# Optimization experiments

Measured on AMD Instinct MI355X. Metric: run time of the kernel, lower is better.

Reference implementation:

```python
import jax, jax.numpy as jnp
import numpy as np

EPS = 1e-3   # Keras BatchNormalization default epsilon
DT = 0.2     # dt
K = 2        # PDE time steps


def _bn(x, p):
    # p: [4, C] = (gamma, beta, moving_mean, moving_var); inference-mode BN
    g, b, m, v = p
    return g * (x - m) * jax.lax.rsqrt(v + EPS) + b


def _dw(x, k):
    # depthwise 3x3 'same' conv; x: NHWC, k: (3,3,1,C)
    return jax.lax.conv_general_dilated(
        x, k, window_strides=(1, 1), padding='SAME',
        dimension_numbers=('NHWC', 'HWIO', 'NHWC'),
        feature_group_count=x.shape[-1])


def setup_inputs() -> dict:
    key = jax.random.key(0)
    ks = jax.random.split(key, 10)
    B, H, W, C = 16, 128, 128, 64
    x = jax.random.normal(ks[0], (B, H, W, C), jnp.float32)

    def kern(k):
        return jax.random.normal(k, (3, 3, 1, C), jnp.float32) * 0.1

    def bnp(k):
        k1, k2, k3, k4 = jax.random.split(k, 4)
        return jnp.stack([
            1.0 + 0.1 * jax.random.normal(k1, (C,), jnp.float32),  # gamma
            0.1 * jax.random.normal(k2, (C,), jnp.float32),        # beta
            0.1 * jax.random.normal(k3, (C,), jnp.float32),        # moving_mean
            0.5 + jax.random.uniform(k4, (C,), jnp.float32),       # moving_var > 0
        ])

    return {
        's0': x,
        'kg': kern(ks[1]), 'kg1': kern(ks[2]),
        'kDx': kern(ks[3]), 'kDy': kern(ks[4]),
        'bng': bnp(ks[5]), 'bng1': bnp(ks[6]),
        'bnDx': bnp(ks[7]), 'bnDy': bnp(ks[8]),
        'bn_out': bnp(ks[9]),
    }


def reference(s0, kg, kg1, kDx, kDy, bng, bng1, bnDx, bnDy, bn_out):
    # init_h is identity ('default' block_type); stride==1, in_chs==out_chs
    f = s0
    h = f
    h0 = f
    g = jax.nn.relu(_bn(_dw(h, kg), bng))
    g1 = jax.nn.relu(_bn(_dw(h, kg1), bng1))
    Dx = jax.nn.relu(_bn(_dw(h, kDx), bnDx))
    Dy = jax.nn.relu(_bn(_dw(h, kDy), bnDy))
    # dx = dy = 1; rolls on axis 2 and 3 exactly as in the TF code (NHWC)
    ux = 0.5 * (jnp.roll(g, 1, axis=2) - jnp.roll(g, -1, axis=2))
    vy = 0.5 * (jnp.roll(g1, 1, axis=3) - jnp.roll(g1, -1, axis=3))
    Ax = g * DT
    Ay = g1 * DT
    Bx = Dx * DT
    By = Dy * DT
    E = (ux + vy) * DT
    D = 1.0 / (1.0 + 2.0 * Bx + 2.0 * By)
    for _ in range(K):
        prev_h = h
        h = D * ((1.0 - 2.0 * Bx - 2.0 * By) * h0
                 - 2.0 * E * h
                 + (-Ax + 2.0 * Bx) * jnp.roll(h, 1, axis=2)
                 + (Ax + 2.0 * Bx) * jnp.roll(h, -1, axis=2)
                 + (-Ay + 2.0 * By) * jnp.roll(h, 1, axis=3)
                 + (Ay + 2.0 * By) * jnp.roll(h, -1, axis=3))
        h = h + D * (2.0 * DT) * f
        h0 = prev_h
    return jax.nn.relu(_bn(h, bn_out))
```

## Files before the change

kernel.cpp:

```cpp
#include <hip/hip_runtime.h>

#define HH 128
#define WW 128
#define CC 64
#define BS 512
#define RS (WW * CC)
#define NPT 4
#define NSTRIP 32

typedef float f4 __attribute__((ext_vector_type(4)));

static __device__ __forceinline__ f4 vload(const float* __restrict__ p) {
    return *reinterpret_cast<const f4*>(p);
}
static __device__ __forceinline__ void vstore(float* p, f4 v) {
    *reinterpret_cast<f4*>(p) = v;
}
static __device__ __forceinline__ f4 vrelu(f4 a) {
    f4 r;
    #pragma unroll
    for (int i = 0; i < 4; ++i) r[i] = fmaxf(a[i], 0.f);
    return r;
}
static __device__ __forceinline__ f4 vrsq_eps(f4 a) {
    f4 r;
    #pragma unroll
    for (int i = 0; i < 4; ++i) r[i] = __builtin_amdgcn_rsqf(a[i] + 1e-3f);
    return r;
}
static __device__ __forceinline__ f4 vrcp(f4 a) {
    f4 r;
    #pragma unroll
    for (int i = 0; i < 4; ++i) r[i] = __builtin_amdgcn_rcpf(a[i]);
    return r;
}

static __device__ __forceinline__ void croll(f4 v, int lm, int lp, f4& cm, f4& cp) {
    const float m3 = __shfl(v.w, lm);
    const float p0 = __shfl(v.x, lp);
    cm.x = m3;  cm.y = v.x; cm.z = v.y; cm.w = v.z;
    cp.x = v.y; cp.y = v.z; cp.z = v.w; cp.w = p0;
}

__global__ __launch_bounds__(BS) void diffusion_fused(
    const float* __restrict__ s0,
    const float* __restrict__ kg,  const float* __restrict__ kg1,
    const float* __restrict__ kDx, const float* __restrict__ kDy,
    const float* __restrict__ bng,  const float* __restrict__ bng1,
    const float* __restrict__ bnDx, const float* __restrict__ bnDy,
    const float* __restrict__ bn_out,
    float* __restrict__ out)
{
    __shared__ float GH[2 * NSTRIP * CC];
    __shared__ float FH[2 * NSTRIP * CC];
    __shared__ float HHb[2 * NSTRIP * CC];

    const int t  = threadIdx.x;
    const int cq = t & 15;
    const int c4 = cq << 2;
    const int s  = t >> 4;
    const int w0 = s << 2;
    const int l  = t & 63;
    const int lm = (l & 48) | ((l + 15) & 15);
    const int lp = (l & 48) | ((l + 1)  & 15);
    const int sl = (s + NSTRIP - 1) & (NSTRIP - 1);
    const int sr = (s + 1) & (NSTRIP - 1);

    const int bid = blockIdx.x;
    const int bh  = ((bid & 7) << 8) | (bid >> 3);
    const int hrow = bh & (HH - 1);
    const long rowbase = (long)bh * RS;
    const bool rowm = (hrow > 0), rowp = (hrow < HH - 1);

    const bool zl = (s == 0), zr = (s == NSTRIP - 1);
    int oc[6];
    oc[0] = (zl ? 0 : (w0 - 1)) * CC + c4;
    #pragma unroll
    for (int j = 1; j <= 4; ++j) oc[j] = (w0 + j - 1) * CC + c4;
    oc[5] = (zr ? (WW - 1) : (w0 + 4)) * CC + c4;

    #define BNFOLD(P, S, B, SC) { \
        const f4 ga  = vload((P) + c4);        \
        const f4 be  = vload((P) + 64 + c4);   \
        const f4 mu  = vload((P) + 128 + c4);  \
        const f4 va  = vload((P) + 192 + c4);  \
        const f4 sc0 = ga * vrsq_eps(va);      \
        S = sc0 * (SC);                        \
        B = (be - mu * sc0) * (SC); }

    f4 s_g, b_g, s_g1, b_g1;
    BNFOLD(bng,  s_g,  b_g,  1.0f);
    BNFOLD(bng1, s_g1, b_g1, 1.0f);

    f4 ag[NPT], ag1[NPT];
    #pragma unroll
    for (int i = 0; i < NPT; ++i) { ag[i] = (f4)0.f; ag1[i] = (f4)0.f; }

    #pragma unroll
    for (int dh = -1; dh <= 1; ++dh) {
        if (dh == -1 && !rowm) continue;
        if (dh ==  1 && !rowp) continue;
        const float* rp = s0 + rowbase + (long)dh * RS;
        f4 in[6];
        #pragma unroll
        for (int j = 0; j < 6; ++j) in[j] = vload(rp + oc[j]);
        if (zl) in[0] = (f4)0.f;
        if (zr) in[5] = (f4)0.f;
        #pragma unroll
        for (int dw = 0; dw < 3; ++dw) {
            const int kk = (dh + 1) * 3 + dw;
            const f4 wg  = vload(kg  + kk * CC + c4);
            const f4 wg1 = vload(kg1 + kk * CC + c4);
            #pragma unroll
            for (int i = 0; i < NPT; ++i) {
                ag[i]  += in[dw + i] * wg;
                ag1[i] += in[dw + i] * wg1;
            }
        }
    }

    f4 g[NPT], g1[NPT];
    #pragma unroll
    for (int i = 0; i < NPT; ++i) {
        g[i]  = vrelu(ag[i]  * s_g  + b_g );
        g1[i] = vrelu(ag1[i] * s_g1 + b_g1);
    }
    vstore(&GH[s * CC + c4],            g[0]);
    vstore(&GH[(NSTRIP + s) * CC + c4], g[NPT - 1]);

    f4 s_dx, b_dx, s_dy, b_dy;
    BNFOLD(bnDx, s_dx, b_dx, 0.4f);
    BNFOLD(bnDy, s_dy, b_dy, 0.4f);

    f4 adx[NPT], ady[NPT], h[NPT];
    #pragma unroll
    for (int i = 0; i < NPT; ++i) { adx[i] = (f4)0.f; ady[i] = (f4)0.f; }

    #pragma unroll
    for (int dh = -1; dh <= 1; ++dh) {
        if (dh == -1 && !rowm) continue;
        if (dh ==  1 && !rowp) continue;
        const float* rp = s0 + rowbase + (long)dh * RS;
        f4 in[6];
        #pragma unroll
        for (int j = 0; j < 6; ++j) in[j] = vload(rp + oc[j]);
        if (zl) in[0] = (f4)0.f;
        if (zr) in[5] = (f4)0.f;
        if (dh == 0) {
            #pragma unroll
            for (int i = 0; i < NPT; ++i) h[i] = in[i + 1];
        }
        #pragma unroll
        for (int dw = 0; dw < 3; ++dw) {
            const int kk = (dh + 1) * 3 + dw;
            const f4 wdx = vload(kDx + kk * CC + c4);
            const f4 wdy = vload(kDy + kk * CC + c4);
            #pragma unroll
            for (int i = 0; i < NPT; ++i) {
                adx[i] += in[dw + i] * wdx;
                ady[i] += in[dw + i] * wdy;
            }
        }
    }
    vstore(&FH[s * CC + c4],            h[0]);
    vstore(&FH[(NSTRIP + s) * CC + c4], h[NPT - 1]);

    f4 cWm[NPT], cWp[NPT], cCm[NPT], cCp[NPT], A0[NPT], PqD[NPT], uv[NPT];
    #pragma unroll
    for (int i = 0; i < NPT; ++i) {
        const f4 tbx = vrelu(adx[i] * s_dx + b_dx);
        const f4 tby = vrelu(ady[i] * s_dy + b_dy);
        const f4 Dv  = vrcp((f4)1.f + tbx + tby);
        const f4 Ax  = g[i]  * 0.2f;
        const f4 Ay  = g1[i] * 0.2f;
        cWm[i] = Dv * (tbx - Ax);
        cWp[i] = Dv * (tbx + Ax);
        cCm[i] = Dv * (tby - Ay);
        cCp[i] = Dv * (tby + Ay);
        A0[i]  = Dv * h[i] * ((f4)1.4f - tbx - tby);
        PqD[i] = Dv * (-0.4f);
        f4 cm, cp;
        croll(g1[i], lm, lp, cm, cp);
        uv[i] = 0.5f * (cm - cp);
    }
    uv[0] -= 0.5f * g[1];
    uv[1] += 0.5f * (g[0] - g[2]);
    uv[2] += 0.5f * (g[1] - g[3]);
    uv[3] += 0.5f * g[2];
    __syncthreads();

    f4 cE[NPT];
    {
        const f4 gL = vload(&GH[(NSTRIP + sl) * CC + c4]);
        const f4 gR = vload(&GH[sr * CC + c4]);
        cE[0] = PqD[0] * (uv[0] + 0.5f * gL);
        cE[1] = PqD[1] * uv[1];
        cE[2] = PqD[2] * uv[2];
        cE[3] = PqD[3] * (uv[3] - 0.5f * gR);
    }

    f4 hn[NPT];
    {
        const f4 hL = vload(&FH[(NSTRIP + sl) * CC + c4]);
        const f4 hR = vload(&FH[sr * CC + c4]);
        #pragma unroll
        for (int i = 0; i < NPT; ++i) {
            const f4 hm = (i == 0)       ? hL : h[i - 1];
            const f4 hp = (i == NPT - 1) ? hR : h[i + 1];
            f4 cm, cp;
            croll(h[i], lm, lp, cm, cp);
            hn[i] = A0[i] + cE[i] * h[i] + cWm[i] * hm + cWp[i] * hp
                  + cCm[i] * cm + cCp[i] * cp;
        }
    }
    vstore(&HHb[s * CC + c4],            hn[0]);
    vstore(&HHb[(NSTRIP + s) * CC + c4], hn[NPT - 1]);
    __syncthreads();

    f4 h2v[NPT];
    {
        const f4 hL = vload(&HHb[(NSTRIP + sl) * CC + c4]);
        const f4 hR = vload(&HHb[sr * CC + c4]);
        #pragma unroll
        for (int i = 0; i < NPT; ++i) {
            const f4 hm = (i == 0)       ? hL : hn[i - 1];
            const f4 hp = (i == NPT - 1) ? hR : hn[i + 1];
            f4 cm, cp;
            croll(hn[i], lm, lp, cm, cp);
            h2v[i] = A0[i] + cE[i] * hn[i] + cWm[i] * hm + cWp[i] * hp
                   + cCm[i] * cm + cCp[i] * cp;
        }
    }

    f4 s_o, b_o;
    BNFOLD(bn_out, s_o, b_o, 1.0f);
    #undef BNFOLD
    #pragma unroll
    for (int i = 0; i < NPT; ++i)
        vstore(out + rowbase + oc[i + 1], vrelu(h2v[i] * s_o + b_o));
}

extern "C" void kernel_launch(void* const* d_in, const int* in_sizes, int n_in,
                              void* d_out, int out_size, void* d_ws, size_t ws_size,
                              hipStream_t stream) {
    const float* s0   = (const float*)d_in[0];
    const float* kg   = (const float*)d_in[1];
    const float* kg1  = (const float*)d_in[2];
    const float* kDx  = (const float*)d_in[3];
    const float* kDy  = (const float*)d_in[4];
    const float* bng  = (const float*)d_in[5];
    const float* bng1 = (const float*)d_in[6];
    const float* bnDx = (const float*)d_in[7];
    const float* bnDy = (const float*)d_in[8];
    const float* bno  = (const float*)d_in[9];
    float* out = (float*)d_out;

    dim3 grid(16 * 128);
    dim3 block(BS);
    diffusion_fused<<<grid, block, 0, stream>>>(
        s0, kg, kg1, kDx, kDy, bng, bng1, bnDx, bnDy, bno, out);
}
```

Measured before the change: 171.3 us.

## Process 8 rows per block with LDS ring buffer and async global-to-LDS staging

Each block now handles eight consecutive image rows instead of one, staging input rows into a three-slot LDS ring through global_load_lds so each input row is fetched once per block rather than three times. Conv weights and folded BN parameters are cached in LDS once per block, and all four depthwise convs are merged into a single pass. This cuts redundant global reads and per-block setup. In exchange it adds per-row barriers, much larger LDS use and a grid of only 256 blocks, which may limit occupancy and latency hiding.

```diff
diff --git a/kernel.cpp b/kernel.cpp
--- a/kernel.cpp
+++ b/kernel.cpp
@@ -7,10 +7,11 @@
 #define RS (WW * CC)
 #define NPT 4
 #define NSTRIP 32
+#define ROWS 8
 
 typedef float f4 __attribute__((ext_vector_type(4)));
 
-static __device__ __forceinline__ f4 vload(const float* __restrict__ p) {
+static __device__ __forceinline__ f4 vload(const float* p) {
     return *reinterpret_cast<const f4*>(p);
 }
 static __device__ __forceinline__ void vstore(float* p, f4 v) {
@@ -34,12 +35,58 @@
     for (int i = 0; i < 4; ++i) r[i] = __builtin_amdgcn_rcpf(a[i]);
     return r;
 }
-
 static __device__ __forceinline__ void croll(f4 v, int lm, int lp, f4& cm, f4& cp) {
     const float m3 = __shfl(v.w, lm);
     const float p0 = __shfl(v.x, lp);
     cm.x = m3;  cm.y = v.x; cm.z = v.y; cm.w = v.z;
     cp.x = v.y; cp.y = v.z; cp.z = v.w; cp.w = p0;
+}
+
+static __device__ __forceinline__ void gld_lds16(const float* g, float* l) {
+    __builtin_amdgcn_global_load_lds(
+        (const __attribute__((address_space(1))) void*)g,
+        (__attribute__((address_space(3))) void*)l,
+        16, 0, 0);
+}
+static __device__ __forceinline__ void stage_row(const float* g, float* l,
+                                                 int wv, int ln) {
+    #pragma unroll
+    for (int it = 0; it < 4; ++it) {
+        const int off = (it * 8 + wv) * 256;
+        gld_lds16(g + off + ln * 4, l + off);
+    }
+}
+
+template<bool CENTER>
+static __device__ __forceinline__ void conv_taps(
+    const float* R, const float* WTS, int kbase, const int* oc,
+    bool zl, bool zr, int c4,
+    f4* ag, f4* ag1, f4* adx, f4* ady, f4* h)
+{
+    f4 in[6];
+    #pragma unroll
+    for (int jj = 0; jj < 6; ++jj) in[jj] = vload(R + oc[jj]);
+    if (zl) in[0] = (f4)0.f;
+    if (zr) in[5] = (f4)0.f;
+    if (CENTER) {
+        #pragma unroll
+        for (int i = 0; i < NPT; ++i) h[i] = in[i + 1];
+    }
+    #pragma unroll
+    for (int dw = 0; dw < 3; ++dw) {
+        const int kk = kbase + dw;
+        const f4 wg  = vload(WTS + (0 * 9 + kk) * CC + c4);
+        const f4 wg1 = vload(WTS + (1 * 9 + kk) * CC + c4);
+        const f4 wdx = vload(WTS + (2 * 9 + kk) * CC + c4);
+        const f4 wdy = vload(WTS + (3 * 9 + kk) * CC + c4);
+        #pragma unroll
+        for (int i = 0; i < NPT; ++i) {
+            ag[i]  += in[dw + i] * wg;
+            ag1[i] += in[dw + i] * wg1;
+            adx[i] += in[dw + i] * wdx;
+            ady[i] += in[dw + i] * wdy;
+        }
+    }
 }
 
 __global__ __launch_bounds__(BS) void diffusion_fused(
@@ -51,9 +98,11 @@
     const float* __restrict__ bn_out,
     float* __restrict__ out)
 {
-    __shared__ float GH[2 * NSTRIP * CC];
-    __shared__ float FH[2 * NSTRIP * CC];
-    __shared__ float HHb[2 * NSTRIP * CC];
+    __shared__ __attribute__((aligned(16))) float ring[3][RS];
+    __shared__ __attribute__((aligned(16))) float GH[2 * NSTRIP * CC];
+    __shared__ __attribute__((aligned(16))) float HHb[2 * NSTRIP * CC];
+    __shared__ __attribute__((aligned(16))) float WTS[4 * 9 * CC];
+    __shared__ __attribute__((aligned(16))) float BNF[10 * CC];
 
     const int t  = threadIdx.x;
     const int cq = t & 15;
@@ -61,16 +110,16 @@
     const int s  = t >> 4;
     const int w0 = s << 2;
     const int l  = t & 63;
+    const int wv = t >> 6;
     const int lm = (l & 48) | ((l + 15) & 15);
     const int lp = (l & 48) | ((l + 1)  & 15);
     const int sl = (s + NSTRIP - 1) & (NSTRIP - 1);
     const int sr = (s + 1) & (NSTRIP - 1);
 
     const int bid = blockIdx.x;
-    const int bh  = ((bid & 7) << 8) | (bid >> 3);
-    const int hrow = bh & (HH - 1);
-    const long rowbase = (long)bh * RS;
-    const bool rowm = (hrow > 0), rowp = (hrow < HH - 1);
+    const int img = bid >> 4;
+    const int r0  = (bid & 15) << 3;
+    const long imgbase = (long)img * HH * RS;
 
     const bool zl = (s == 0), zr = (s == NSTRIP - 1);
     int oc[6];
@@ -78,166 +127,151 @@
     #pragma unroll
     for (int j = 1; j <= 4; ++j) oc[j] = (w0 + j - 1) * CC + c4;
     oc[5] = (zr ? (WW - 1) : (w0 + 4)) * CC + c4;
-
-    #define BNFOLD(P, S, B, SC) { \
-        const f4 ga  = vload((P) + c4);        \
-        const f4 be  = vload((P) + 64 + c4);   \
-        const f4 mu  = vload((P) + 128 + c4);  \
-        const f4 va  = vload((P) + 192 + c4);  \
-        const f4 sc0 = ga * vrsq_eps(va);      \
-        S = sc0 * (SC);                        \
-        B = (be - mu * sc0) * (SC); }
-
-    f4 s_g, b_g, s_g1, b_g1;
-    BNFOLD(bng,  s_g,  b_g,  1.0f);
-    BNFOLD(bng1, s_g1, b_g1, 1.0f);
-
-    f4 ag[NPT], ag1[NPT];
-    #pragma unroll
-    for (int i = 0; i < NPT; ++i) { ag[i] = (f4)0.f; ag1[i] = (f4)0.f; }
-
-    #pragma unroll
-    for (int dh = -1; dh <= 1; ++dh) {
-        if (dh == -1 && !rowm) continue;
-        if (dh ==  1 && !rowp) continue;
-        const float* rp = s0 + rowbase + (long)dh * RS;
-        f4 in[6];
-        #pragma unroll
-        for (int j = 0; j < 6; ++j) in[j] = vload(rp + oc[j]);
-        if (zl) in[0] = (f4)0.f;
-        if (zr) in[5] = (f4)0.f;
-        #pragma unroll
-        for (int dw = 0; dw < 3; ++dw) {
-            const int kk = (dh + 1) * 3 + dw;
-            const f4 wg  = vload(kg  + kk * CC + c4);
-            const f4 wg1 = vload(kg1 + kk * CC + c4);
+    const int wmo = ((w0 - 1) & (WW - 1)) * CC + c4;
+    const int wpo = ((w0 + 4) & (WW - 1)) * CC + c4;
+
+    if (r0 > 0)
+        stage_row(s0 + imgbase + (long)(r0 - 1) * RS, ring[(r0 - 1) % 3], wv, l);
+    stage_row(s0 + imgbase + (long)r0 * RS,       ring[r0 % 3],       wv, l);
+    stage_row(s0 + imgbase + (long)(r0 + 1) * RS, ring[(r0 + 1) % 3], wv, l);
+
+    {
+        const float* wsrc[4] = { kg, kg1, kDx, kDy };
+        #pragma unroll
+        for (int base = 0; base < 576; base += BS) {
+            const int slot = base + t;
+            if (slot < 576) {
+                const int q   = slot / 144;
+                const int rem = slot - q * 144;
+                const int kk  = rem >> 4;
+                const int cc4 = (rem & 15) << 2;
+                vstore(&WTS[(q * 9 + kk) * CC + cc4], vload(wsrc[q] + kk * CC + cc4));
+            }
+        }
+    }
+    if (s == 0) {
+        #define BNF1(P, K, SC) { \
+            const f4 ga = vload((P) + c4);       const f4 be = vload((P) + 64 + c4);  \
+            const f4 mu = vload((P) + 128 + c4); const f4 va = vload((P) + 192 + c4); \
+            const f4 sc0 = ga * vrsq_eps(va);                                         \
+            vstore(&BNF[(2 * (K)) * CC + c4], sc0 * (SC));                            \
+            vstore(&BNF[(2 * (K) + 1) * CC + c4], (be - mu * sc0) * (SC)); }
+        BNF1(bng,    0, 1.0f);
+        BNF1(bng1,   1, 1.0f);
+        BNF1(bnDx,   2, 0.4f);
+        BNF1(bnDy,   3, 0.4f);
+        BNF1(bn_out, 4, 1.0f);
+        #undef BNF1
+    }
+    __syncthreads();
+
+    for (int j = 0; j < ROWS; ++j) {
+        const int gr = r0 + j;
+        const bool rowm = (gr > 0), rowp = (gr < HH - 1);
+        const float* Rm = ring[(gr + 2) % 3];
+        const float* Rc = ring[gr % 3];
+        const float* Rp = ring[(gr + 1) % 3];
+
+        f4 ag[NPT], ag1[NPT], adx[NPT], ady[NPT], h[NPT];
+        #pragma unroll
+        for (int i = 0; i < NPT; ++i) {
+            ag[i] = (f4)0.f; ag1[i] = (f4)0.f; adx[i] = (f4)0.f; ady[i] = (f4)0.f;
+        }
+
+        if (rowm) conv_taps<false>(Rm, WTS, 0, oc, zl, zr, c4, ag, ag1, adx, ady, h);
+        __syncthreads();
+        if (j < ROWS - 1 && gr + 2 < HH)
+            stage_row(s0 + imgbase + (long)(gr + 2) * RS, ring[(gr + 2) % 3], wv, l);
+
+        conv_taps<true >(Rc, WTS, 3, oc, zl, zr, c4, ag, ag1, adx, ady, h);
+        if (rowp) conv_taps<false>(Rp, WTS, 6, oc, zl, zr, c4, ag, ag1, adx, ady, h);
+
+        const f4 s_g  = vload(&BNF[0 * CC + c4]), b_g  = vload(&BNF[1 * CC + c4]);
+        const f4 s_g1 = vload(&BNF[2 * CC + c4]), b_g1 = vload(&BNF[3 * CC + c4]);
+        const f4 s_dx = vload(&BNF[4 * CC + c4]), b_dx = vload(&BNF[5 * CC + c4]);
+        const f4 s_dy = vload(&BNF[6 * CC + c4]), b_dy = vload(&BNF[7 * CC + c4]);
+        f4 g[NPT], g1[NPT];
+        #pragma unroll
+        for (int i = 0; i < NPT; ++i) {
+            g[i]  = vrelu(ag[i]  * s_g  + b_g );
+            g1[i] = vrelu(ag1[i] * s_g1 + b_g1);
+        }
+        vstore(&GH[s * CC + c4],            g[0]);
+        vstore(&GH[(NSTRIP + s) * CC + c4], g[NPT - 1]);
+
+        f4 cWm[NPT], cWp[NPT], cCm[NPT], cCp[NPT], A0[NPT], PqD[NPT], uv[NPT];
+        #pragma unroll
+        for (int i = 0; i < NPT; ++i) {
+            const f4 tbx = vrelu(adx[i] * s_dx + b_dx);
+            const f4 tby = vrelu(ady[i] * s_dy + b_dy);
+            const f4 Dv  = vrcp((f4)1.f + tbx + tby);
+            const f4 Ax  = g[i]  * 0.2f;
+            const f4 Ay  = g1[i] * 0.2f;
+            cWm[i] = Dv * (tbx - Ax);
+            cWp[i] = Dv * (tbx + Ax);
+            cCm[i] = Dv * (tby - Ay);
+            cCp[i] = Dv * (tby + Ay);
+            A0[i]  = Dv * h[i] * ((f4)1.4f - tbx - tby);
+            PqD[i] = Dv * (-0.4f);
+            f4 cm, cp;
+            croll(g1[i], lm, lp, cm, cp);
+            uv[i] = 0.5f * (cm - cp);
+        }
+        uv[0] -= 0.5f * g[1];
+        uv[1] += 0.5f * (g[0] - g[2]);
+        uv[2] += 0.5f * (g[1] - g[3]);
+        uv[3] += 0.5f * g[2];
+        __syncthreads();
+
+        f4 cE[NPT];
+        {
+            const f4 gL = vload(&GH[(NSTRIP + sl) * CC + c4]);
+            const f4 gR = vload(&GH[sr * CC + c4]);
+            cE[0] = PqD[0] * (uv[0] + 0.5f * gL);
+            cE[1] = PqD[1] * uv[1];
+            cE[2] = PqD[2] * uv[2];
+            cE[3] = PqD[3] * (uv[3] - 0.5f * gR);
+        }
+
+        f4 hn[NPT];
+        {
+            const f4 hL = vload(Rc + wmo);
+            const f4 hR = vload(Rc + wpo);
             #pragma unroll
             for (int i = 0; i < NPT; ++i) {
-                ag[i]  += in[dw + i] * wg;
-                ag1[i] += in[dw + i] * wg1;
+                const f4 hm = (i == 0)       ? hL : h[i - 1];
+                const f4 hp = (i == NPT - 1) ? hR : h[i + 1];
+                f4 cm, cp;
+                croll(h[i], lm, lp, cm, cp);
+                hn[i] = A0[i] + cE[i] * h[i] + cWm[i] * hm + cWp[i] * hp
+                      + cCm[i] * cm + cCp[i] * cp;
             }
         }
-    }
-
-    f4 g[NPT], g1[NPT];
-    #pragma unroll
-    for (int i = 0; i < NPT; ++i) {
-        g[i]  = vrelu(ag[i]  * s_g  + b_g );
-        g1[i] = vrelu(ag1[i] * s_g1 + b_g1);
-    }
-    vstore(&GH[s * CC + c4],            g[0]);
-    vstore(&GH[(NSTRIP + s) * CC + c4], g[NPT - 1]);
-
-    f4 s_dx, b_dx, s_dy, b_dy;
-    BNFOLD(bnDx, s_dx, b_dx, 0.4f);
-    BNFOLD(bnDy, s_dy, b_dy, 0.4f);
-
-    f4 adx[NPT], ady[NPT], h[NPT];
-    #pragma unroll
-    for (int i = 0; i < NPT; ++i) { adx[i] = (f4)0.f; ady[i] = (f4)0.f; }
-
-    #pragma unroll
-    for (int dh = -1; dh <= 1; ++dh) {
-        if (dh == -1 && !rowm) continue;
-        if (dh ==  1 && !rowp) continue;
-        const float* rp = s0 + rowbase + (long)dh * RS;
-        f4 in[6];
-        #pragma unroll
-        for (int j = 0; j < 6; ++j) in[j] = vload(rp + oc[j]);
-        if (zl) in[0] = (f4)0.f;
-        if (zr) in[5] = (f4)0.f;
-        if (dh == 0) {
-            #pragma unroll
-            for (int i = 0; i < NPT; ++i) h[i] = in[i + 1];
-        }
-        #pragma unroll
-        for (int dw = 0; dw < 3; ++dw) {
-            const int kk = (dh + 1) * 3 + dw;
-            const f4 wdx = vload(kDx + kk * CC + c4);
-            const f4 wdy = vload(kDy + kk * CC + c4);
+        vstore(&HHb[s * CC + c4],            hn[0]);
+        vstore(&HHb[(NSTRIP + s) * CC + c4], hn[NPT - 1]);
+        __syncthreads();
+
+        f4 h2v[NPT];
+        {
+            const f4 hL = vload(&HHb[(NSTRIP + sl) * CC + c4]);
+            const f4 hR = vload(&HHb[sr * CC + c4]);
             #pragma unroll
             for (int i = 0; i < NPT; ++i) {
-                adx[i] += in[dw + i] * wdx;
-                ady[i] += in[dw + i] * wdy;
+                const f4 hm = (i == 0)       ? hL : hn[i - 1];
+                const f4 hp = (i == NPT - 1) ? hR : hn[i + 1];
+                f4 cm, cp;
+                croll(hn[i], lm, lp, cm, cp);
+                h2v[i] = A0[i] + cE[i] * hn[i] + cWm[i] * hm + cWp[i] * hp
+                       + cCm[i] * cm + cCp[i] * cp;
             }
         }
-    }
-    vstore(&FH[s * CC + c4],            h[0]);
-    vstore(&FH[(NSTRIP + s) * CC + c4], h[NPT - 1]);
-
-    f4 cWm[NPT], cWp[NPT], cCm[NPT], cCp[NPT], A0[NPT], PqD[NPT], uv[NPT];
-    #pragma unroll
-    for (int i = 0; i < NPT; ++i) {
-        const f4 tbx = vrelu(adx[i] * s_dx + b_dx);
-        const f4 tby = vrelu(ady[i] * s_dy + b_dy);
-        const f4 Dv  = vrcp((f4)1.f + tbx + tby);
-        const f4 Ax  = g[i]  * 0.2f;
-        const f4 Ay  = g1[i] * 0.2f;
-        cWm[i] = Dv * (tbx - Ax);
-        cWp[i] = Dv * (tbx + Ax);
-        cCm[i] = Dv * (tby - Ay);
-        cCp[i] = Dv * (tby + Ay);
-        A0[i]  = Dv * h[i] * ((f4)1.4f - tbx - tby);
-        PqD[i] = Dv * (-0.4f);
-        f4 cm, cp;
-        croll(g1[i], lm, lp, cm, cp);
-        uv[i] = 0.5f * (cm - cp);
-    }
-    uv[0] -= 0.5f * g[1];
-    uv[1] += 0.5f * (g[0] - g[2]);
-    uv[2] += 0.5f * (g[1] - g[3]);
-    uv[3] += 0.5f * g[2];
-    __syncthreads();
-
-    f4 cE[NPT];
-    {
-        const f4 gL = vload(&GH[(NSTRIP + sl) * CC + c4]);
-        const f4 gR = vload(&GH[sr * CC + c4]);
-        cE[0] = PqD[0] * (uv[0] + 0.5f * gL);
-        cE[1] = PqD[1] * uv[1];
-        cE[2] = PqD[2] * uv[2];
-        cE[3] = PqD[3] * (uv[3] - 0.5f * gR);
-    }
-
-    f4 hn[NPT];
-    {
-        const f4 hL = vload(&FH[(NSTRIP + sl) * CC + c4]);
-        const f4 hR = vload(&FH[sr * CC + c4]);
-        #pragma unroll
-        for (int i = 0; i < NPT; ++i) {
-            const f4 hm = (i == 0)       ? hL : h[i - 1];
-            const f4 hp = (i == NPT - 1) ? hR : h[i + 1];
-            f4 cm, cp;
-            croll(h[i], lm, lp, cm, cp);
-            hn[i] = A0[i] + cE[i] * h[i] + cWm[i] * hm + cWp[i] * hp
-                  + cCm[i] * cm + cCp[i] * cp;
-        }
-    }
-    vstore(&HHb[s * CC + c4],            hn[0]);
-    vstore(&HHb[(NSTRIP + s) * CC + c4], hn[NPT - 1]);
-    __syncthreads();
-
-    f4 h2v[NPT];
-    {
-        const f4 hL = vload(&HHb[(NSTRIP + sl) * CC + c4]);
-        const f4 hR = vload(&HHb[sr * CC + c4]);
-        #pragma unroll
-        for (int i = 0; i < NPT; ++i) {
-            const f4 hm = (i == 0)       ? hL : hn[i - 1];
-            const f4 hp = (i == NPT - 1) ? hR : hn[i + 1];
-            f4 cm, cp;
-            croll(hn[i], lm, lp, cm, cp);
-            h2v[i] = A0[i] + cE[i] * hn[i] + cWm[i] * hm + cWp[i] * hp
-                   + cCm[i] * cm + cCp[i] * cp;
-        }
-    }
-
-    f4 s_o, b_o;
-    BNFOLD(bn_out, s_o, b_o, 1.0f);
-    #undef BNFOLD
-    #pragma unroll
-    for (int i = 0; i < NPT; ++i)
-        vstore(out + rowbase + oc[i + 1], vrelu(h2v[i] * s_o + b_o));
+
+        const f4 s_o = vload(&BNF[8 * CC + c4]), b_o = vload(&BNF[9 * CC + c4]);
+        const long rowout = imgbase + (long)gr * RS;
+        #pragma unroll
+        for (int i = 0; i < NPT; ++i)
+            vstore(out + rowout + oc[i + 1], vrelu(h2v[i] * s_o + b_o));
+    }
 }
 
 extern "C" void kernel_launch(void* const* d_in, const int* in_sizes, int n_in,
@@ -255,7 +289,7 @@
     const float* bno  = (const float*)d_in[9];
     float* out = (float*)d_out;
 
-    dim3 grid(16 * 128);
+    dim3 grid(16 * (HH / ROWS));
     dim3 block(BS);
     diffusion_fused<<<grid, block, 0, stream>>>(
         s0, kg, kg1, kDx, kDy, bng, bng1, bnDx, bnDy, bno, out);
```

Result: faster. 151.1 us (-11.8%).
